# Optimization experiments

Measured on AMD Instinct MI355X. Metric: run time of the kernel, lower is better.

The kernel has to match this reference:

```python
import jax, jax.numpy as jnp
import numpy as np

# iRPE config: ratio=1.9, method='euc', mode='ctx', shared_head=True, skip=1, rpe_on='k'
ALPHA, BETA, GAMMA = 1.9, 3.8, 15.2  # alpha=1*ratio, beta=2*ratio, gamma=8*ratio
NUM_HEADS = 12


def _rp_bucket_euc(height, width, skip):
    """Static relative-position bucket ids (Euclidean method, piecewise index).
    Returns (skip+L, skip+L) int array and num_buckets."""
    coords = np.stack(np.meshgrid(np.arange(height), np.arange(width), indexing='ij'), -1)
    coords = coords.reshape(-1, 2).astype(np.float64)  # (L, 2)
    diff = coords[:, None, :] - coords[None, :, :]      # (L, L, 2)
    dis = np.round(np.sqrt((diff ** 2).sum(-1)))        # (L, L), nonnegative
    # piecewise_index: identity for dis<=alpha, log-spaced (rounded, clipped at beta) beyond
    log_idx = np.minimum(
        np.round(ALPHA + np.log(np.maximum(dis, 1e-9) / ALPHA) / np.log(GAMMA / ALPHA) * (BETA - ALPHA)),
        BETA).astype(np.int64)
    bucket = np.where(dis <= ALPHA, np.round(dis).astype(np.int64), log_idx)
    bucket = bucket - bucket.min()
    nb = 2 * int(BETA) + 1  # 7
    if skip > 0:
        L = height * width
        full = np.full((skip + L, skip + L), nb, dtype=np.int64)  # extra bucket for cls token
        full[skip:, skip:] = bucket
        bucket, nb = full, nb + 1  # nb = 8
    return jnp.asarray(bucket), nb


def setup_inputs() -> dict:
    key = jax.random.key(0)
    ks = jax.random.split(key, 4)
    B, N, C = 8, 1025, 768  # 32x32 patches + 1 cls token
    hd = C // NUM_HEADS
    nb = 2 * int(BETA) + 1 + 1  # 8 buckets (incl. skip bucket)
    return {
        "x": jax.random.normal(ks[0], (B, N, C), jnp.float32),
        "qkv_w": jax.random.normal(ks[1], (3 * C, C), jnp.float32) * 0.02,
        "proj_w": jax.random.normal(ks[2], (C, C), jnp.float32) * 0.02,
        "proj_b": jnp.zeros((C,), jnp.float32),
        "rpe_w": jax.random.normal(ks[3], (hd, nb), jnp.float32) * 0.02,  # shared across heads
    }


def reference(x, qkv_w, proj_w, proj_b, rpe_w):
    B, N, C = x.shape
    H = NUM_HEADS
    hd = C // H
    scale = hd ** -0.5
    n_modalities = 1
    height = int((N // n_modalities) ** 0.5)        # 32 (mask is None path)
    skip = N - n_modalities * height * height       # 1 (cls token)
    rp_bucket, _ = _rp_bucket_euc(height, height, skip)  # (N, N) int, static

    qkv = (x @ qkv_w.T).reshape(B, N, 3, H, hd).transpose(2, 0, 3, 1, 4)  # (3,B,H,N,hd)
    q, k, v = qkv[0] * scale, qkv[1], qkv[2]
    attn = jnp.einsum('bhid,bhjd->bhij', q, k)
    # contextual RPE on keys (shared head): bias[b,h,i,j] = q[b,h,i,:] @ rpe_w[:, bucket[i,j]]
    lookup = jnp.einsum('bhid,dm->bhim', q, rpe_w)                      # (B,H,N,nb)
    bias = jnp.take_along_axis(lookup, rp_bucket[None, None, :, :], axis=3)  # (B,H,N,N)
    attn = jax.nn.softmax(attn + bias, axis=-1)
    out = jnp.einsum('bhij,bhjd->bhid', attn, v)
    out = out.transpose(0, 2, 1, 3).reshape(B, N, C)
    return out @ proj_w.T + proj_b
```

## Files before the change

### kernel.cpp

```cpp
#include <hip/hip_runtime.h>
#include <math.h>

#define B_    8
#define N_    1025
#define H_    12
#define HD_   64
#define C_    768
#define BH_   (B_*H_)
#define NTOK  (B_*N_)
#define SCALE 0.125f
#define NPAD  1092
#define NPADV 1088

#define QKV_ELEMS (BH_*N_*HD_)

#define XB_OFF_B     ((size_t)0)
#define WQKV_OFF_B   (XB_OFF_B + (size_t)NTOK*C_*2)
#define WPROJ_OFF_B  (WQKV_OFF_B + (size_t)3*C_*C_*2)
#define QB_OFF_B     (WPROJ_OFF_B + (size_t)C_*C_*2)
#define KB_OFF_B     (QB_OFF_B + (size_t)QKV_ELEMS*2)
#define AOB_OFF_B    (KB_OFF_B + (size_t)QKV_ELEMS*2)
#define VT_OFF_B     (AOB_OFF_B + (size_t)QKV_ELEMS*2)
#define BUCKET_OFF_B (VT_OFF_B + (size_t)BH_*HD_*NPADV*2)

typedef __attribute__((ext_vector_type(8))) short s8bf;
typedef __attribute__((ext_vector_type(8))) unsigned short u8s;
typedef __attribute__((ext_vector_type(4))) float v4f;
typedef unsigned short ushort_t;

#define GLOAD16(gp, lp) __builtin_amdgcn_global_load_lds( \
    (const __attribute__((address_space(1))) unsigned int*)(gp), \
    (__attribute__((address_space(3))) unsigned int*)(lp), 16, 0, 0)

#define SBAR() do { \
    __builtin_amdgcn_sched_barrier(0); \
    asm volatile("s_barrier" ::: "memory"); \
    __builtin_amdgcn_sched_barrier(0); \
} while (0)

__device__ __forceinline__ unsigned short f2bf(float x) {
    union { float f; unsigned u; } v; v.f = x;
    unsigned r = v.u + 0x7FFFu + ((v.u >> 16) & 1u);
    return (unsigned short)(r >> 16);
}
__device__ __forceinline__ unsigned packbf_hu(float lo, float hi) {
    union { float f; unsigned u; } a, b; a.f = lo; b.f = hi;
    return ((a.u + 0x8000u) >> 16) | ((b.u + 0x8000u) & 0xFFFF0000u);
}

__global__ void bucket_kernel(unsigned char* __restrict__ bucketT) {
    int tid = blockIdx.x * 256 + threadIdx.x;
    if (tid >= N_ * NPAD) return;
    unsigned ut = (unsigned)tid;
    int j = ut / (unsigned)NPAD, i = ut % (unsigned)NPAD;
    if (i >= N_) i = N_ - 1;
    int bk;
    if (i < 1 || j < 1) {
        bk = 7;
    } else {
        int pi = i - 1, pj = j - 1;
        int dy = (pi >> 5) - (pj >> 5);
        int dx = (pi & 31) - (pj & 31);
        int d2 = dy*dy + dx*dx;
        bk = (d2 == 0) ? 0 : ((d2 <= 2) ? 1 : ((d2 <= 12) ? 2 : 3));
    }
    bucketT[tid] = (unsigned char)bk;
}

__global__ __launch_bounds__(256) void cast_kernel(
        const float* __restrict__ x, const float* __restrict__ w1,
        const float* __restrict__ w2,
        ushort_t* __restrict__ xb, ushort_t* __restrict__ w1b,
        ushort_t* __restrict__ w2b) {
    const int NX = NTOK * C_ / 8, NW1 = 3 * C_ * C_ / 8, NW2 = C_ * C_ / 8;
    int g = blockIdx.x * 256 + threadIdx.x;
    const float* src; ushort_t* dst; int idx;
    if (g < NX)                 { src = x;  dst = xb;  idx = g; }
    else if (g < NX + NW1)      { src = w1; dst = w1b; idx = g - NX; }
    else if (g < NX + NW1 + NW2){ src = w2; dst = w2b; idx = g - NX - NW1; }
    else return;
    size_t off = (size_t)idx * 8;
    float4 a = *(const float4*)(src + off);
    float4 c = *(const float4*)(src + off + 4);
    __align__(16) ushort_t h[8] = {f2bf(a.x), f2bf(a.y), f2bf(a.z), f2bf(a.w),
                                   f2bf(c.x), f2bf(c.y), f2bf(c.z), f2bf(c.w)};
    *(u8s*)(dst + off) = *(u8s*)h;
}

__global__ __launch_bounds__(256) void qkv_kernel(
        const ushort_t* __restrict__ xb, const ushort_t* __restrict__ wb,
        ushort_t* __restrict__ qb, ushort_t* __restrict__ kb, ushort_t* __restrict__ vt) {
    __shared__ __align__(16) ushort_t As0[128*64];
    __shared__ __align__(16) ushort_t Bs0[128*64];
    __shared__ __align__(16) ushort_t As1[128*64];
    __shared__ __align__(16) ushort_t Bs1[128*64];
    const int L = blockIdx.x + blockIdx.y * 65;
    const int xcd = L & 7, idx = L >> 3;
    const int wg = (xcd < 2 ? xcd * 147 : 2 * 147 + (xcd - 2) * 146) + idx;
    const int m0 = (wg / 18) * 128, c0 = (wg % 18) * 128;
    const int t = threadIdx.x;
    const int w = t >> 6, lane = t & 63, lc = lane & 15, lq = lane >> 4;
    const int wm = (w >> 1) * 64, wn = (w & 1) * 64;
    const int srow8 = w * 32 + (lane >> 3);
    const int gsw8  = (((lane & 7) ^ (lane >> 3)) & 7) * 8;

    v4f acc[4][4];
#pragma unroll
    for (int mt = 0; mt < 4; mt++)
#pragma unroll
        for (int nt = 0; nt < 4; nt++) acc[mt][nt] = (v4f){0.f, 0.f, 0.f, 0.f};

    auto STAGE = [&](ushort_t* Ad, ushort_t* Bd, int k0) {
#pragma unroll
        for (int i = 0; i < 4; i++) {
            int row = srow8 + i * 8;
            int m = m0 + row; if (m > NTOK - 1) m = NTOK - 1;
            GLOAD16(xb + (size_t)m * C_ + k0 + gsw8,           &Ad[(w*32 + i*8) * 64]);
            GLOAD16(wb + (size_t)(c0 + row) * C_ + k0 + gsw8,  &Bd[(w*32 + i*8) * 64]);
        }
    };
    auto COMPUTE = [&](const ushort_t* A, const ushort_t* B) {
#pragma unroll
        for (int kk = 0; kk < 64; kk += 32) {
            s8bf af[4], bf[4];
#pragma unroll
            for (int mt = 0; mt < 4; mt++)
                af[mt] = *(const s8bf*)&A[(wm + mt*16 + lc) * 64 + ((((kk>>3) + lq) ^ (lc & 7)) * 8)];
#pragma unroll
            for (int nt = 0; nt < 4; nt++)
                bf[nt] = *(const s8bf*)&B[(wn + nt*16 + lc) * 64 + ((((kk>>3) + lq) ^ (lc & 7)) * 8)];
#pragma unroll
            for (int mt = 0; mt < 4; mt++)
#pragma unroll
                for (int nt = 0; nt < 4; nt++)
                    acc[mt][nt] = __builtin_amdgcn_mfma_f32_16x16x32_bf16(af[mt], bf[nt], acc[mt][nt], 0, 0, 0);
        }
    };

    STAGE(As0, Bs0, 0);
#pragma unroll
    for (int it = 0; it < 6; ++it) {
        const int k0 = it * 128;
        if (k0 + 64 < C_) {
            STAGE(As1, Bs1, k0 + 64);
            asm volatile("s_waitcnt vmcnt(8)" ::: "memory");
        } else {
            asm volatile("s_waitcnt vmcnt(0)" ::: "memory");
        }
        SBAR();
        COMPUTE(As0, Bs0);
        SBAR();
        if (k0 + 128 < C_) {
            STAGE(As0, Bs0, k0 + 128);
            asm volatile("s_waitcnt vmcnt(8)" ::: "memory");
        } else {
            asm volatile("s_waitcnt vmcnt(0)" ::: "memory");
        }
        SBAR();
        COMPUTE(As1, Bs1);
        if (it < 5) SBAR();
    }

#pragma unroll
    for (int mt = 0; mt < 4; mt++) {
#pragma unroll
        for (int r = 0; r < 4; r++) {
            int m = m0 + wm + mt*16 + lq*4 + r;
            if (m >= NTOK) continue;
            unsigned um = (unsigned)m;
            int b = um / (unsigned)N_, n = um % (unsigned)N_;
#pragma unroll
            for (int nt = 0; nt < 4; nt++) {
                int c = c0 + wn + nt*16 + lc;
                int comp = c / C_, rem = c % C_;
                int h = rem >> 6, d0 = rem & 63;
                float val = acc[mt][nt][r] * ((comp == 0) ? SCALE : 1.0f);
                if (comp == 2) {
                    vt[((size_t)((b*H_ + h)*HD_ + d0))*NPADV + n] = f2bf(val);
                } else {
                    ushort_t* dst = (comp == 0) ? qb : kb;
                    dst[((size_t)((b*H_ + h)*N_ + n))*HD_ + d0] = f2bf(val);
                }
            }
        }
    }
}

#define LUTS 9

__global__ __launch_bounds__(256) void attn_kernel(
        const ushort_t* __restrict__ qb, const ushort_t* __restrict__ kb,
        const ushort_t* __restrict__ vt, const float* __restrict__ rpe,
        const unsigned char* __restrict__ bucketT, ushort_t* __restrict__ ao) {
    __shared__ __align__(16) ushort_t Ks[64*64];
    __shared__ __align__(16) ushort_t Vs[64*64];
    __shared__ float lut[64*LUTS];

    const int bh = blockIdx.x, it = blockIdx.y;
    const int b  = bh / H_, hh = bh % H_;
    const int i0 = it * 64;
    const int t  = threadIdx.x;
    const int w  = t >> 6, lane = t & 63, lc = lane & 15, lq = lane >> 4;
    const int row_w = w * 16;
    const int rs = lc & 7;
    const int gA = ((lq ^ rs) & 7) * 8;
    const int gB = (((lq + 4) ^ rs) & 7) * 8;

    const ushort_t* qp = qb + (size_t)bh * N_ * HD_;
    const ushort_t* kp = kb + (size_t)bh * N_ * HD_;
    const ushort_t* vp = vt + (size_t)bh * HD_ * NPADV;

    {
        int row = t >> 2, g0 = (t & 3) * 2, qrs = row & 7;
        int gi = i0 + row;
        u8s h0 = (u8s)0, h1 = (u8s)0;
        if (gi < N_) {
            h0 = *(const u8s*)(qp + (size_t)gi * HD_ + g0*8);
            h1 = *(const u8s*)(qp + (size_t)gi * HD_ + g0*8 + 8);
        }
        *(u8s*)&Vs[row*64 + ((g0 ^ qrs) * 8)]       = h0;
        *(u8s*)&Vs[row*64 + (((g0+1) ^ qrs) * 8)]   = h1;
    }
    if (t < 64) {
        float4 r0 = *(const float4*)(rpe + t*8);
        float4 r1 = *(const float4*)(rpe + t*8 + 4);
        const int gr = t >> 3, go = t & 7;
        float vals[8] = {r0.x, r0.y, r0.z, r0.w, r1.x, r1.y, r1.z, r1.w};
#pragma unroll
        for (int m = 0; m < 8; m++)
            Ks[m*64 + ((gr ^ (m & 7)) * 8) + go] = f2bf(vals[m]);
    } else if (t < 128) {
        int idx = t - 64;
        int m = 8 + (idx >> 3), g = idx & 7;
        *(u8s*)&Ks[m*64 + ((g ^ (m & 7)) * 8)] = (u8s)0;
    }
    __syncthreads();

    s8bf qf0 = *(s8bf*)&Vs[(row_w + lc)*64 + gA];
    s8bf qf1 = *(s8bf*)&Vs[(row_w + lc)*64 + gB];

    {
        s8bf rf0 = *(s8bf*)&Ks[lc*64 + gA];
        s8bf rf1 = *(s8bf*)&Ks[lc*64 + gB];
        v4f la = (v4f){0.f, 0.f, 0.f, 0.f};
        la = __builtin_amdgcn_mfma_f32_16x16x32_bf16(qf0, rf0, la, 0, 0, 0);
        la = __builtin_amdgcn_mfma_f32_16x16x32_bf16(qf1, rf1, la, 0, 0, 0);
        if (lc < 8) {
#pragma unroll
            for (int r = 0; r < 4; r++)
                lut[(row_w + lq*4 + r)*LUTS + lc] = la[r];
        }
    }

    const int srow = t >> 2, g0 = (t & 3) * 2, sd0 = g0 * 8;
    const int kslot = ((srow >> 5) * 2 + ((srow >> 2) & 1)) * 16 + ((srow >> 3) & 3) * 4 + (srow & 3);
    const int krs = kslot & 7, vrs = srow & 7;
    ushort_t* const kd0 = &Ks[kslot*64 + ((g0 ^ krs) * 8)];
    ushort_t* const kd1 = &Ks[kslot*64 + (((g0+1) ^ krs) * 8)];
    ushort_t* const vd0 = &Vs[srow*64 + ((g0 ^ vrs) * 8)];
    ushort_t* const vd1 = &Vs[srow*64 + (((g0+1) ^ vrs) * 8)];
    u8s krg0, krg1, vrg0, vrg1;
    {
        const ushort_t* ks = kp + (size_t)srow * HD_ + sd0;
        krg0 = *(const u8s*)ks; krg1 = *(const u8s*)(ks + 8);
        const ushort_t* vs = vp + (size_t)srow * NPADV + sd0;
        vrg0 = *(const u8s*)vs; vrg1 = *(const u8s*)(vs + 8);
    }
    int myrow = i0 + row_w + lc; if (myrow > N_ - 1) myrow = N_ - 1;
    const unsigned char* bkrow = bucketT + (size_t)myrow * NPAD;
    const int lutbase = (row_w + lc) * LUTS;
    const int jb0 = 8*lq, jb1 = 8*lq + 4, jb2 = 8*lq + 32, jb3 = 8*lq + 36;
    unsigned bk4[4];
    bk4[0] = *(const unsigned*)(bkrow + jb0);
    bk4[1] = *(const unsigned*)(bkrow + jb1);
    bk4[2] = *(const unsigned*)(bkrow + jb2);
    bk4[3] = *(const unsigned*)(bkrow + jb3);

    v4f o[4];
    float lsum = 0.f;
#pragma unroll
    for (int dt = 0; dt < 4; dt++) o[dt] = (v4f){0.f, 0.f, 0.f, 0.f};

    for (int jt = 0; jt < 16; jt++) {
        const int j0 = jt * 64;
        __syncthreads();
        {
            *(u8s*)kd0 = krg0; *(u8s*)kd1 = krg1;
            *(u8s*)vd0 = vrg0; *(u8s*)vd1 = vrg1;
        }
        __syncthreads();

        unsigned bk4n[4];
        {
            int gj = j0 + 64 + srow; if (gj > N_ - 1) gj = N_ - 1;
            const ushort_t* ks = kp + (size_t)gj * HD_ + sd0;
            krg0 = *(const u8s*)ks; krg1 = *(const u8s*)(ks + 8);
            const ushort_t* vs = vp + (size_t)srow * NPADV + (j0 + 64) + sd0;
            vrg0 = *(const u8s*)vs; vrg1 = *(const u8s*)(vs + 8);
            bk4n[0] = *(const unsigned*)(bkrow + j0 + 64 + jb0);
            bk4n[1] = *(const unsigned*)(bkrow + j0 + 64 + jb1);
            bk4n[2] = *(const unsigned*)(bkrow + j0 + 64 + jb2);
            bk4n[3] = *(const unsigned*)(bkrow + j0 + 64 + jb3);
        }

        v4f acc[4];
#pragma unroll
        for (int t4 = 0; t4 < 4; t4++) acc[t4] = (v4f){0.f, 0.f, 0.f, 0.f};
#pragma unroll
        for (int t4 = 0; t4 < 4; t4++) {
            s8bf kf0 = *(s8bf*)&Ks[(t4*16 + lc)*64 + gA];
            s8bf kf1 = *(s8bf*)&Ks[(t4*16 + lc)*64 + gB];
            acc[t4] = __builtin_amdgcn_mfma_f32_16x16x32_bf16(kf0, qf0, acc[t4], 0, 0, 0);
            acc[t4] = __builtin_amdgcn_mfma_f32_16x16x32_bf16(kf1, qf1, acc[t4], 0, 0, 0);
        }

        unsigned pw[8];
#pragma unroll
        for (int t4 = 0; t4 < 4; t4++) {
            float p0, p1, p2, p3;
            {
                int k0b = (bk4[t4]      ) & 0xFF; p0 = __expf(acc[t4][0] + lut[lutbase + k0b]);
                int k1b = (bk4[t4] >>  8) & 0xFF; p1 = __expf(acc[t4][1] + lut[lutbase + k1b]);
                int k2b = (bk4[t4] >> 16) & 0xFF; p2 = __expf(acc[t4][2] + lut[lutbase + k2b]);
                int k3b = (bk4[t4] >> 24)       ; p3 = __expf(acc[t4][3] + lut[lutbase + k3b]);
            }
            lsum += (p0 + p1) + (p2 + p3);
            pw[t4*2]     = packbf_hu(p0, p1);
            pw[t4*2 + 1] = packbf_hu(p2, p3);
        }
#pragma unroll
        for (int t4 = 0; t4 < 4; t4++) bk4[t4] = bk4n[t4];
        s8bf pf0 = *(s8bf*)&pw[0];
        s8bf pf1 = *(s8bf*)&pw[4];

#pragma unroll
        for (int dt = 0; dt < 4; dt++) {
            s8bf vf0 = *(s8bf*)&Vs[(dt*16 + lc)*64 + gA];
            s8bf vf1 = *(s8bf*)&Vs[(dt*16 + lc)*64 + gB];
            o[dt] = __builtin_amdgcn_mfma_f32_16x16x32_bf16(pf0, vf0, o[dt], 0, 0, 0);
            o[dt] = __builtin_amdgcn_mfma_f32_16x16x32_bf16(pf1, vf1, o[dt], 0, 0, 0);
        }
    }

    {
        __syncthreads();
        {
            *(u8s*)kd0 = krg0; *(u8s*)kd1 = krg1;
            *(u8s*)vd0 = vrg0; *(u8s*)vd1 = vrg1;
        }
        __syncthreads();

        v4f acc[4];
#pragma unroll
        for (int t4 = 0; t4 < 4; t4++) acc[t4] = (v4f){0.f, 0.f, 0.f, 0.f};
#pragma unroll
        for (int t4 = 0; t4 < 4; t4++) {
            s8bf kf0 = *(s8bf*)&Ks[(t4*16 + lc)*64 + gA];
            s8bf kf1 = *(s8bf*)&Ks[(t4*16 + lc)*64 + gB];
            acc[t4] = __builtin_amdgcn_mfma_f32_16x16x32_bf16(kf0, qf0, acc[t4], 0, 0, 0);
            acc[t4] = __builtin_amdgcn_mfma_f32_16x16x32_bf16(kf1, qf1, acc[t4], 0, 0, 0);
        }

        unsigned pw[8];
        const int jbs[4] = {jb0, jb1, jb2, jb3};
#pragma unroll
        for (int t4 = 0; t4 < 4; t4++) {
            float pv[4];
#pragma unroll
            for (int r = 0; r < 4; r++) {
                int bk = (bk4[t4] >> (8*r)) & 0xFF;
                float p = __expf(acc[t4][r] + lut[lutbase + bk]);
                if ((jbs[t4] + r) > 0) p = 0.f;
                lsum += p;
                pv[r] = p;
            }
            pw[t4*2]     = packbf_hu(pv[0], pv[1]);
            pw[t4*2 + 1] = packbf_hu(pv[2], pv[3]);
        }
        s8bf pf0 = *(s8bf*)&pw[0];
        s8bf pf1 = *(s8bf*)&pw[4];
#pragma unroll
        for (int dt = 0; dt < 4; dt++) {
            s8bf vf0 = *(s8bf*)&Vs[(dt*16 + lc)*64 + gA];
            s8bf vf1 = *(s8bf*)&Vs[(dt*16 + lc)*64 + gB];
            o[dt] = __builtin_amdgcn_mfma_f32_16x16x32_bf16(pf0, vf0, o[dt], 0, 0, 0);
            o[dt] = __builtin_amdgcn_mfma_f32_16x16x32_bf16(pf1, vf1, o[dt], 0, 0, 0);
        }
    }

    lsum += __shfl_xor(lsum, 16);
    lsum += __shfl_xor(lsum, 32);
    if (lq == 0) lut[(row_w + lc)*LUTS + 8] = lsum;
    __builtin_amdgcn_s_waitcnt(0);
#pragma unroll
    for (int r = 0; r < 4; r++) {
        int i = i0 + row_w + lq*4 + r;
        if (i < N_) {
            float inv = 1.0f / lut[(row_w + lq*4 + r)*LUTS + 8];
#pragma unroll
            for (int dt = 0; dt < 4; dt++)
                ao[((size_t)(b*N_ + i))*C_ + hh*HD_ + dt*16 + lc] = f2bf(o[dt][r] * inv);
        }
    }
}

__global__ __launch_bounds__(256) void proj_kernel(
        const ushort_t* __restrict__ ab, const ushort_t* __restrict__ wb,
        const float* __restrict__ bias, float* __restrict__ out) {
    __shared__ __align__(16) ushort_t As0[128*64];
    __shared__ __align__(16) ushort_t Bs0[128*64];
    __shared__ __align__(16) ushort_t As1[128*64];
    __shared__ __align__(16) ushort_t Bs1[128*64];
    const int L = blockIdx.x + blockIdx.y * 65;
    const int xcd = L & 7, idx = L >> 3;
    const int wg = (xcd < 6 ? xcd * 49 : 6 * 49 + (xcd - 6) * 48) + idx;
    const int m0 = (wg / 6) * 128, c0 = (wg % 6) * 128;
    const int t = threadIdx.x;
    const int w = t >> 6, lane = t & 63, lc = lane & 15, lq = lane >> 4;
    const int wm = (w >> 1) * 64, wn = (w & 1) * 64;
    const int srow8 = w * 32 + (lane >> 3);
    const int gsw8  = (((lane & 7) ^ (lane >> 3)) & 7) * 8;

    v4f acc[4][4];
#pragma unroll
    for (int mt = 0; mt < 4; mt++)
#pragma unroll
        for (int nt = 0; nt < 4; nt++) acc[mt][nt] = (v4f){0.f, 0.f, 0.f, 0.f};

    auto STAGE = [&](ushort_t* Ad, ushort_t* Bd, int k0) {
#pragma unroll
        for (int i = 0; i < 4; i++) {
            int row = srow8 + i * 8;
            int m = m0 + row; if (m > NTOK - 1) m = NTOK - 1;
            GLOAD16(ab + (size_t)m * C_ + k0 + gsw8,           &Ad[(w*32 + i*8) * 64]);
            GLOAD16(wb + (size_t)(c0 + row) * C_ + k0 + gsw8,  &Bd[(w*32 + i*8) * 64]);
        }
    };
    auto COMPUTE = [&](const ushort_t* A, const ushort_t* B) {
#pragma unroll
        for (int kk = 0; kk < 64; kk += 32) {
            s8bf af[4], bf[4];
#pragma unroll
            for (int mt = 0; mt < 4; mt++)
                af[mt] = *(const s8bf*)&A[(wm + mt*16 + lc) * 64 + ((((kk>>3) + lq) ^ (lc & 7)) * 8)];
#pragma unroll
            for (int nt = 0; nt < 4; nt++)
                bf[nt] = *(const s8bf*)&B[(wn + nt*16 + lc) * 64 + ((((kk>>3) + lq) ^ (lc & 7)) * 8)];
#pragma unroll
            for (int mt = 0; mt < 4; mt++)
#pragma unroll
                for (int nt = 0; nt < 4; nt++)
                    acc[mt][nt] = __builtin_amdgcn_mfma_f32_16x16x32_bf16(af[mt], bf[nt], acc[mt][nt], 0, 0, 0);
        }
    };

    STAGE(As0, Bs0, 0);
#pragma unroll
    for (int it = 0; it < 6; ++it) {
        const int k0 = it * 128;
        if (k0 + 64 < C_) {
            STAGE(As1, Bs1, k0 + 64);
            asm volatile("s_waitcnt vmcnt(8)" ::: "memory");
        } else {
            asm volatile("s_waitcnt vmcnt(0)" ::: "memory");
        }
        SBAR();
        COMPUTE(As0, Bs0);
        SBAR();
        if (k0 + 128 < C_) {
            STAGE(As0, Bs0, k0 + 128);
            asm volatile("s_waitcnt vmcnt(8)" ::: "memory");
        } else {
            asm volatile("s_waitcnt vmcnt(0)" ::: "memory");
        }
        SBAR();
        COMPUTE(As1, Bs1);
        if (it < 5) SBAR();
    }

    float pb[4];
#pragma unroll
    for (int nt = 0; nt < 4; nt++) pb[nt] = bias[c0 + wn + nt*16 + lc];
#pragma unroll
    for (int mt = 0; mt < 4; mt++) {
#pragma unroll
        for (int r = 0; r < 4; r++) {
            int m = m0 + wm + mt*16 + lq*4 + r;
            if (m >= NTOK) continue;
#pragma unroll
            for (int nt = 0; nt < 4; nt++) {
                int c = c0 + wn + nt*16 + lc;
                out[(size_t)m * C_ + c] = acc[mt][nt][r] + pb[nt];
            }
        }
    }
}

extern "C" void kernel_launch(void* const* d_in, const int* in_sizes, int n_in,
                              void* d_out, int out_size, void* d_ws, size_t ws_size,
                              hipStream_t stream) {
    const float* x      = (const float*)d_in[0];
    const float* qkv_w  = (const float*)d_in[1];
    const float* proj_w = (const float*)d_in[2];
    const float* proj_b = (const float*)d_in[3];
    const float* rpe_w  = (const float*)d_in[4];
    float* out = (float*)d_out;

    char* ws = (char*)d_ws;
    ushort_t* xb   = (ushort_t*)(ws + XB_OFF_B);
    ushort_t* wqkv = (ushort_t*)(ws + WQKV_OFF_B);
    ushort_t* wprj = (ushort_t*)(ws + WPROJ_OFF_B);
    ushort_t* qb   = (ushort_t*)(ws + QB_OFF_B);
    ushort_t* kb   = (ushort_t*)(ws + KB_OFF_B);
    ushort_t* aob  = (ushort_t*)(ws + AOB_OFF_B);
    ushort_t* vt   = (ushort_t*)(ws + VT_OFF_B);
    unsigned char* bucketT = (unsigned char*)(ws + BUCKET_OFF_B);

    const int ncast = (NTOK*C_ + 3*C_*C_ + C_*C_) / 8;
    bucket_kernel<<<dim3((N_*NPAD + 255)/256), 256, 0, stream>>>(bucketT);
    cast_kernel<<<dim3((ncast + 255)/256), 256, 0, stream>>>(x, qkv_w, proj_w, xb, wqkv, wprj);
    qkv_kernel<<<dim3(65, 18), 256, 0, stream>>>(xb, wqkv, qb, kb, vt);
    attn_kernel<<<dim3(96, 17), 256, 0, stream>>>(qb, kb, vt, rpe_w, bucketT, aob);
    proj_kernel<<<dim3(65, 6), 256, 0, stream>>>(aob, wprj, proj_b, out);
}
```

Before: 225.5 us.

## Double-buffer K/V tiles in LDS using direct global-to-LDS async loads

Replaces the register-staged K/V prefetch (global load to VGPRs, then LDS store between two __syncthreads) with global_load_lds direct copies into ping-pong LDS buffers. The next tile is issued before the current one is computed, guarded by explicit vmcnt waits and raw s_barriers. This aims to overlap global memory latency with MFMA/exp work and drop one barrier plus the VGPR round trip per tile. In exchange LDS use doubles, which may reduce occupancy, and the hand-tuned vmcnt counts and swizzled source addressing must exactly match the old layout for correctness.

```diff
diff --git a/kernel.cpp b/kernel.cpp
--- a/kernel.cpp
+++ b/kernel.cpp
@@ -35,6 +35,11 @@
 #define SBAR() do { \
     __builtin_amdgcn_sched_barrier(0); \
     asm volatile("s_barrier" ::: "memory"); \
+    __builtin_amdgcn_sched_barrier(0); \
+} while (0)
+#define VMW(N) do { \
+    __builtin_amdgcn_sched_barrier(0); \
+    asm volatile("s_waitcnt vmcnt(" #N ")" ::: "memory"); \
     __builtin_amdgcn_sched_barrier(0); \
 } while (0)
 
@@ -192,13 +197,15 @@
         const ushort_t* __restrict__ qb, const ushort_t* __restrict__ kb,
         const ushort_t* __restrict__ vt, const float* __restrict__ rpe,
         const unsigned char* __restrict__ bucketT, ushort_t* __restrict__ ao) {
-    __shared__ __align__(16) ushort_t Ks[64*64];
-    __shared__ __align__(16) ushort_t Vs[64*64];
+    __shared__ __align__(16) ushort_t Ks0[64*64];
+    __shared__ __align__(16) ushort_t Vs0[64*64];
+    __shared__ __align__(16) ushort_t Ks1[64*64];
+    __shared__ __align__(16) ushort_t Vs1[64*64];
     __shared__ float lut[64*LUTS];
 
-    const int bh = blockIdx.x, it = blockIdx.y;
+    const int bh = blockIdx.x, it0 = blockIdx.y;
     const int b  = bh / H_, hh = bh % H_;
-    const int i0 = it * 64;
+    const int i0 = it0 * 64;
     const int t  = threadIdx.x;
     const int w  = t >> 6, lane = t & 63, lc = lane & 15, lq = lane >> 4;
     const int row_w = w * 16;
@@ -218,8 +225,8 @@
             h0 = *(const u8s*)(qp + (size_t)gi * HD_ + g0*8);
             h1 = *(const u8s*)(qp + (size_t)gi * HD_ + g0*8 + 8);
         }
-        *(u8s*)&Vs[row*64 + ((g0 ^ qrs) * 8)]       = h0;
-        *(u8s*)&Vs[row*64 + (((g0+1) ^ qrs) * 8)]   = h1;
+        *(u8s*)&Vs1[row*64 + ((g0 ^ qrs) * 8)]       = h0;
+        *(u8s*)&Vs1[row*64 + (((g0+1) ^ qrs) * 8)]   = h1;
     }
     if (t < 64) {
         float4 r0 = *(const float4*)(rpe + t*8);
@@ -228,20 +235,20 @@
         float vals[8] = {r0.x, r0.y, r0.z, r0.w, r1.x, r1.y, r1.z, r1.w};
 #pragma unroll
         for (int m = 0; m < 8; m++)
-            Ks[m*64 + ((gr ^ (m & 7)) * 8) + go] = f2bf(vals[m]);
+            Ks1[m*64 + ((gr ^ (m & 7)) * 8) + go] = f2bf(vals[m]);
     } else if (t < 128) {
         int idx = t - 64;
         int m = 8 + (idx >> 3), g = idx & 7;
-        *(u8s*)&Ks[m*64 + ((g ^ (m & 7)) * 8)] = (u8s)0;
+        *(u8s*)&Ks1[m*64 + ((g ^ (m & 7)) * 8)] = (u8s)0;
     }
     __syncthreads();
 
-    s8bf qf0 = *(s8bf*)&Vs[(row_w + lc)*64 + gA];
-    s8bf qf1 = *(s8bf*)&Vs[(row_w + lc)*64 + gB];
+    s8bf qf0 = *(s8bf*)&Vs1[(row_w + lc)*64 + gA];
+    s8bf qf1 = *(s8bf*)&Vs1[(row_w + lc)*64 + gB];
 
     {
-        s8bf rf0 = *(s8bf*)&Ks[lc*64 + gA];
-        s8bf rf1 = *(s8bf*)&Ks[lc*64 + gB];
+        s8bf rf0 = *(s8bf*)&Ks1[lc*64 + gA];
+        s8bf rf1 = *(s8bf*)&Ks1[lc*64 + gB];
         v4f la = (v4f){0.f, 0.f, 0.f, 0.f};
         la = __builtin_amdgcn_mfma_f32_16x16x32_bf16(qf0, rf0, la, 0, 0, 0);
         la = __builtin_amdgcn_mfma_f32_16x16x32_bf16(qf1, rf1, la, 0, 0, 0);
@@ -252,141 +259,112 @@
         }
     }
 
-    const int srow = t >> 2, g0 = (t & 3) * 2, sd0 = g0 * 8;
-    const int kslot = ((srow >> 5) * 2 + ((srow >> 2) & 1)) * 16 + ((srow >> 3) & 3) * 4 + (srow & 3);
-    const int krs = kslot & 7, vrs = srow & 7;
-    ushort_t* const kd0 = &Ks[kslot*64 + ((g0 ^ krs) * 8)];
-    ushort_t* const kd1 = &Ks[kslot*64 + (((g0+1) ^ krs) * 8)];
-    ushort_t* const vd0 = &Vs[srow*64 + ((g0 ^ vrs) * 8)];
-    ushort_t* const vd1 = &Vs[srow*64 + (((g0+1) ^ vrs) * 8)];
-    u8s krg0, krg1, vrg0, vrg1;
-    {
-        const ushort_t* ks = kp + (size_t)srow * HD_ + sd0;
-        krg0 = *(const u8s*)ks; krg1 = *(const u8s*)(ks + 8);
-        const ushort_t* vs = vp + (size_t)srow * NPADV + sd0;
-        vrg0 = *(const u8s*)vs; vrg1 = *(const u8s*)(vs + 8);
-    }
     int myrow = i0 + row_w + lc; if (myrow > N_ - 1) myrow = N_ - 1;
     const unsigned char* bkrow = bucketT + (size_t)myrow * NPAD;
     const int lutbase = (row_w + lc) * LUTS;
     const int jb0 = 8*lq, jb1 = 8*lq + 4, jb2 = 8*lq + 32, jb3 = 8*lq + 36;
     unsigned bk4[4];
+
+    auto STAGEA = [&](ushort_t* Kd, ushort_t* Vd, int jbase) {
+#pragma unroll
+        for (int i = 0; i < 2; i++) {
+            int s = w*16 + i*8 + (lane >> 3);
+            int jr = 32*(s>>5) + 8*((s>>2)&3) + 4*((s>>4)&1) + (s&3);
+            int gj = jbase + jr; if (gj > N_ - 1) gj = N_ - 1;
+            GLOAD16(kp + (size_t)gj * HD_ + (((lane&7) ^ (s&7)) * 8), &Kd[(w*16 + i*8)*64]);
+        }
+#pragma unroll
+        for (int i = 0; i < 2; i++) {
+            int d = w*16 + i*8 + (lane >> 3);
+            GLOAD16(vp + (size_t)d * NPADV + jbase + (((lane&7) ^ (d&7)) * 8), &Vd[(w*16 + i*8)*64]);
+        }
+    };
+
+    v4f o[4];
+    float lsum = 0.f;
+#pragma unroll
+    for (int dt = 0; dt < 4; dt++) o[dt] = (v4f){0.f, 0.f, 0.f, 0.f};
+
+    auto TILE = [&](const ushort_t* Kb, const ushort_t* Vb, int nextj, bool tail) {
+        v4f acc[4];
+#pragma unroll
+        for (int t4 = 0; t4 < 4; t4++) acc[t4] = (v4f){0.f, 0.f, 0.f, 0.f};
+#pragma unroll
+        for (int t4 = 0; t4 < 4; t4++) {
+            s8bf kf0 = *(const s8bf*)&Kb[(t4*16 + lc)*64 + gA];
+            s8bf kf1 = *(const s8bf*)&Kb[(t4*16 + lc)*64 + gB];
+            acc[t4] = __builtin_amdgcn_mfma_f32_16x16x32_bf16(kf0, qf0, acc[t4], 0, 0, 0);
+            acc[t4] = __builtin_amdgcn_mfma_f32_16x16x32_bf16(kf1, qf1, acc[t4], 0, 0, 0);
+        }
+        unsigned pw[8];
+        if (!tail) {
+#pragma unroll
+            for (int t4 = 0; t4 < 4; t4++) {
+                int k0b = (bk4[t4]      ) & 0xFF; float p0 = __expf(acc[t4][0] + lut[lutbase + k0b]);
+                int k1b = (bk4[t4] >>  8) & 0xFF; float p1 = __expf(acc[t4][1] + lut[lutbase + k1b]);
+                int k2b = (bk4[t4] >> 16) & 0xFF; float p2 = __expf(acc[t4][2] + lut[lutbase + k2b]);
+                int k3b = (bk4[t4] >> 24)       ; float p3 = __expf(acc[t4][3] + lut[lutbase + k3b]);
+                lsum += (p0 + p1) + (p2 + p3);
+                pw[t4*2]     = packbf_hu(p0, p1);
+                pw[t4*2 + 1] = packbf_hu(p2, p3);
+            }
+        } else {
+            const int jbs[4] = {jb0, jb1, jb2, jb3};
+#pragma unroll
+            for (int t4 = 0; t4 < 4; t4++) {
+                float pv[4];
+#pragma unroll
+                for (int r = 0; r < 4; r++) {
+                    int bk = (bk4[t4] >> (8*r)) & 0xFF;
+                    float p = __expf(acc[t4][r] + lut[lutbase + bk]);
+                    if ((jbs[t4] + r) > 0) p = 0.f;
+                    lsum += p;
+                    pv[r] = p;
+                }
+                pw[t4*2]     = packbf_hu(pv[0], pv[1]);
+                pw[t4*2 + 1] = packbf_hu(pv[2], pv[3]);
+            }
+        }
+        if (nextj >= 0) {
+            bk4[0] = *(const unsigned*)(bkrow + nextj + jb0);
+            bk4[1] = *(const unsigned*)(bkrow + nextj + jb1);
+            bk4[2] = *(const unsigned*)(bkrow + nextj + jb2);
+            bk4[3] = *(const unsigned*)(bkrow + nextj + jb3);
+        }
+        s8bf pf0 = *(s8bf*)&pw[0];
+        s8bf pf1 = *(s8bf*)&pw[4];
+#pragma unroll
+        for (int dt = 0; dt < 4; dt++) {
+            s8bf vf0 = *(const s8bf*)&Vb[(dt*16 + lc)*64 + gA];
+            s8bf vf1 = *(const s8bf*)&Vb[(dt*16 + lc)*64 + gB];
+            o[dt] = __builtin_amdgcn_mfma_f32_16x16x32_bf16(pf0, vf0, o[dt], 0, 0, 0);
+            o[dt] = __builtin_amdgcn_mfma_f32_16x16x32_bf16(pf1, vf1, o[dt], 0, 0, 0);
+        }
+    };
+
+    STAGEA(Ks0, Vs0, 0);
     bk4[0] = *(const unsigned*)(bkrow + jb0);
     bk4[1] = *(const unsigned*)(bkrow + jb1);
     bk4[2] = *(const unsigned*)(bkrow + jb2);
     bk4[3] = *(const unsigned*)(bkrow + jb3);
-
-    v4f o[4];
-    float lsum = 0.f;
-#pragma unroll
-    for (int dt = 0; dt < 4; dt++) o[dt] = (v4f){0.f, 0.f, 0.f, 0.f};
-
-    for (int jt = 0; jt < 16; jt++) {
-        const int j0 = jt * 64;
-        __syncthreads();
-        {
-            *(u8s*)kd0 = krg0; *(u8s*)kd1 = krg1;
-            *(u8s*)vd0 = vrg0; *(u8s*)vd1 = vrg1;
-        }
-        __syncthreads();
-
-        unsigned bk4n[4];
-        {
-            int gj = j0 + 64 + srow; if (gj > N_ - 1) gj = N_ - 1;
-            const ushort_t* ks = kp + (size_t)gj * HD_ + sd0;
-            krg0 = *(const u8s*)ks; krg1 = *(const u8s*)(ks + 8);
-            const ushort_t* vs = vp + (size_t)srow * NPADV + (j0 + 64) + sd0;
-            vrg0 = *(const u8s*)vs; vrg1 = *(const u8s*)(vs + 8);
-            bk4n[0] = *(const unsigned*)(bkrow + j0 + 64 + jb0);
-            bk4n[1] = *(const unsigned*)(bkrow + j0 + 64 + jb1);
-            bk4n[2] = *(const unsigned*)(bkrow + j0 + 64 + jb2);
-            bk4n[3] = *(const unsigned*)(bkrow + j0 + 64 + jb3);
-        }
-
-        v4f acc[4];
-#pragma unroll
-        for (int t4 = 0; t4 < 4; t4++) acc[t4] = (v4f){0.f, 0.f, 0.f, 0.f};
-#pragma unroll
-        for (int t4 = 0; t4 < 4; t4++) {
-            s8bf kf0 = *(s8bf*)&Ks[(t4*16 + lc)*64 + gA];
-            s8bf kf1 = *(s8bf*)&Ks[(t4*16 + lc)*64 + gB];
-            acc[t4] = __builtin_amdgcn_mfma_f32_16x16x32_bf16(kf0, qf0, acc[t4], 0, 0, 0);
-            acc[t4] = __builtin_amdgcn_mfma_f32_16x16x32_bf16(kf1, qf1, acc[t4], 0, 0, 0);
-        }
-
-        unsigned pw[8];
-#pragma unroll
-        for (int t4 = 0; t4 < 4; t4++) {
-            float p0, p1, p2, p3;
-            {
-                int k0b = (bk4[t4]      ) & 0xFF; p0 = __expf(acc[t4][0] + lut[lutbase + k0b]);
-                int k1b = (bk4[t4] >>  8) & 0xFF; p1 = __expf(acc[t4][1] + lut[lutbase + k1b]);
-                int k2b = (bk4[t4] >> 16) & 0xFF; p2 = __expf(acc[t4][2] + lut[lutbase + k2b]);
-                int k3b = (bk4[t4] >> 24)       ; p3 = __expf(acc[t4][3] + lut[lutbase + k3b]);
-            }
-            lsum += (p0 + p1) + (p2 + p3);
-            pw[t4*2]     = packbf_hu(p0, p1);
-            pw[t4*2 + 1] = packbf_hu(p2, p3);
-        }
-#pragma unroll
-        for (int t4 = 0; t4 < 4; t4++) bk4[t4] = bk4n[t4];
-        s8bf pf0 = *(s8bf*)&pw[0];
-        s8bf pf1 = *(s8bf*)&pw[4];
-
-#pragma unroll
-        for (int dt = 0; dt < 4; dt++) {
-            s8bf vf0 = *(s8bf*)&Vs[(dt*16 + lc)*64 + gA];
-            s8bf vf1 = *(s8bf*)&Vs[(dt*16 + lc)*64 + gB];
-            o[dt] = __builtin_amdgcn_mfma_f32_16x16x32_bf16(pf0, vf0, o[dt], 0, 0, 0);
-            o[dt] = __builtin_amdgcn_mfma_f32_16x16x32_bf16(pf1, vf1, o[dt], 0, 0, 0);
-        }
-    }
-
-    {
-        __syncthreads();
-        {
-            *(u8s*)kd0 = krg0; *(u8s*)kd1 = krg1;
-            *(u8s*)vd0 = vrg0; *(u8s*)vd1 = vrg1;
-        }
-        __syncthreads();
-
-        v4f acc[4];
-#pragma unroll
-        for (int t4 = 0; t4 < 4; t4++) acc[t4] = (v4f){0.f, 0.f, 0.f, 0.f};
-#pragma unroll
-        for (int t4 = 0; t4 < 4; t4++) {
-            s8bf kf0 = *(s8bf*)&Ks[(t4*16 + lc)*64 + gA];
-            s8bf kf1 = *(s8bf*)&Ks[(t4*16 + lc)*64 + gB];
-            acc[t4] = __builtin_amdgcn_mfma_f32_16x16x32_bf16(kf0, qf0, acc[t4], 0, 0, 0);
-            acc[t4] = __builtin_amdgcn_mfma_f32_16x16x32_bf16(kf1, qf1, acc[t4], 0, 0, 0);
-        }
-
-        unsigned pw[8];
-        const int jbs[4] = {jb0, jb1, jb2, jb3};
-#pragma unroll
-        for (int t4 = 0; t4 < 4; t4++) {
-            float pv[4];
-#pragma unroll
-            for (int r = 0; r < 4; r++) {
-                int bk = (bk4[t4] >> (8*r)) & 0xFF;
-                float p = __expf(acc[t4][r] + lut[lutbase + bk]);
-                if ((jbs[t4] + r) > 0) p = 0.f;
-                lsum += p;
-                pv[r] = p;
-            }
-            pw[t4*2]     = packbf_hu(pv[0], pv[1]);
-            pw[t4*2 + 1] = packbf_hu(pv[2], pv[3]);
-        }
-        s8bf pf0 = *(s8bf*)&pw[0];
-        s8bf pf1 = *(s8bf*)&pw[4];
-#pragma unroll
-        for (int dt = 0; dt < 4; dt++) {
-            s8bf vf0 = *(s8bf*)&Vs[(dt*16 + lc)*64 + gA];
-            s8bf vf1 = *(s8bf*)&Vs[(dt*16 + lc)*64 + gB];
-            o[dt] = __builtin_amdgcn_mfma_f32_16x16x32_bf16(pf0, vf0, o[dt], 0, 0, 0);
-            o[dt] = __builtin_amdgcn_mfma_f32_16x16x32_bf16(pf1, vf1, o[dt], 0, 0, 0);
-        }
-    }
+    SBAR();
+
+    for (int it = 0; it < 8; ++it) {
+        const int j0 = it * 128;
+        STAGEA(Ks1, Vs1, j0 + 64);
+        VMW(4);
+        SBAR();
+        TILE(Ks0, Vs0, j0 + 64, false);
+        SBAR();
+        STAGEA(Ks0, Vs0, j0 + 128);
+        VMW(4);
+        SBAR();
+        TILE(Ks1, Vs1, j0 + 128, false);
+        SBAR();
+    }
+    VMW(0);
+    SBAR();
+    TILE(Ks0, Vs0, -1, true);
 
     lsum += __shfl_xor(lsum, 16);
     lsum += __shfl_xor(lsum, 32);
```

Result: slower. 232.1 us (+2.9%).
